# Kernel tuning notes

Measured on AMD Instinct MI355X. Metric: run time of the kernel, lower is better.

Reference implementation:

```python
import jax, jax.numpy as jnp
import numpy as np

N = 50000
E = 800000
IN_F = 128
HID_F = 128
OUT_F = 128
BN_EPS = 1e-5


def make_quaternion_mul(kernel):
    # kernel: [d_in//4, d_out]; returns hamilton: [d_in, d_out]
    r, i, j, k = jnp.split(kernel, 4, axis=1)
    r2 = jnp.concatenate([r, -i, -j, -k], axis=0)
    i2 = jnp.concatenate([i, r, -k, j], axis=0)
    j2 = jnp.concatenate([j, k, r, -i], axis=0)
    k2 = jnp.concatenate([k, -j, i, r], axis=0)
    return jnp.concatenate([r2, i2, j2, k2], axis=1)


def setup_inputs() -> dict:
    key = jax.random.key(0)
    k1, k2, k3, k4, k5, k6 = jax.random.split(key, 6)
    stdv = np.sqrt(6.0 / (IN_F // 4 + HID_F)).astype(np.float32)
    inputs = {
        "input": jax.random.normal(k1, (N, IN_F), dtype=jnp.float32),
        "adj_row": jnp.sort(jax.random.randint(k2, (E,), 0, N, dtype=jnp.int32)),
        "adj_col": jax.random.randint(k3, (E,), 0, N, dtype=jnp.int32),
        "adj_val": jax.random.uniform(k4, (E,), dtype=jnp.float32),
        "weight1": jax.random.uniform(k5, (IN_F // 4, HID_F), minval=-stdv, maxval=stdv, dtype=jnp.float32),
        "weight2": jax.random.uniform(k6, (HID_F // 4, OUT_F), minval=-stdv, maxval=stdv, dtype=jnp.float32),
        "gamma": jnp.ones((OUT_F,), dtype=jnp.float32),
        "beta": jnp.zeros((OUT_F,), dtype=jnp.float32),
    }
    return inputs


def reference(input, adj_row, adj_col, adj_val, weight1, weight2, gamma, beta):
    hamilton1 = make_quaternion_mul(weight1)  # [IN_F, HID_F]
    hamilton2 = make_quaternion_mul(weight2)  # [HID_F, OUT_F]
    out1 = jnp.tanh(input @ hamilton1)        # [N, HID_F]
    out2 = out1 @ hamilton2                   # [N, OUT_F]
    # sparse adj (COO) x dense: out[i] = sum_e val[e] * out2[col[e]] for row[e]==i
    gathered = adj_val[:, None] * out2[adj_col]  # [E, OUT_F]
    agg = jax.ops.segment_sum(gathered, adj_row, num_segments=N)  # [N, OUT_F]
    # BatchNorm1d (training mode): per-feature stats over nodes, biased var
    mean = jnp.mean(agg, axis=0)
    var = jnp.var(agg, axis=0)
    return gamma * (agg - mean) * jax.lax.rsqrt(var + BN_EPS) + beta
```

## Files before the change

kernel.cpp:

```cpp
#include <hip/hip_runtime.h>
#include <cstddef>
#include <cstdint>

#define F 128
#define LDK 136
#define AGG_BLOCKS 2048
#define MID_BLOCKS 64

typedef __attribute__((ext_vector_type(8))) short short8;
typedef __attribute__((ext_vector_type(4))) float f32x4;

__device__ __forceinline__ short f2bf(float f) {
  uint32_t u = __float_as_uint(f);
  uint32_t r = u + 0x7FFFu + ((u >> 16) & 1u);
  return (short)(r >> 16);
}
__device__ __forceinline__ float bf2f(short h) {
  return __uint_as_float(((uint32_t)(uint16_t)h) << 16);
}

__global__ __launch_bounds__(256) void setup_kernel(
    const float* __restrict__ w1, const float* __restrict__ w2,
    short* __restrict__ Hpk, const int* __restrict__ adj_row,
    const int* __restrict__ adj_col, const float* __restrict__ adj_val,
    int* __restrict__ rowptr, uint2* __restrict__ cv, int E, int N) {
  if (blockIdx.x < 16) {
    int idx = blockIdx.x * 256 + threadIdx.x;
    int m = idx >> 11;
    int kt = (idx >> 9) & 3;
    int ct = (idx >> 6) & 7;
    int l = idx & 63;
    int col = ct * 16 + (l & 15);
    const float* w = m ? w2 : w1;
    short hi[8], lo[8];
#pragma unroll
    for (int j = 0; j < 8; ++j) {
      int row = kt * 32 + (l >> 4) * 8 + j;
      int rb = row >> 5, cb = col >> 5;
      int neg = (0x284E >> (cb * 4 + rb)) & 1;
      float v = w[(row & 31) * 128 + (rb ^ cb) * 32 + (col & 31)];
      v = neg ? -v : v;
      short h = f2bf(v);
      hi[j] = h;
      lo[j] = f2bf(v - bf2f(h));
    }
    size_t b0 = ((((size_t)m * 2 + 0) * 4 + kt) * 8 + ct) * 64 + l;
    size_t b1 = ((((size_t)m * 2 + 1) * 4 + kt) * 8 + ct) * 64 + l;
    *(short8*)&Hpk[b0 * 8] = *(short8*)hi;
    *(short8*)&Hpk[b1 * 8] = *(short8*)lo;
  } else {
    int e = (blockIdx.x - 16) * 256 + threadIdx.x;
    if (e >= E) return;
    cv[e] = make_uint2((uint32_t)adj_col[e], __float_as_uint(adj_val[e]));
    int r = adj_row[e];
    int rprev = (e == 0) ? -1 : adj_row[e - 1];
    for (int q = rprev + 1; q <= r; ++q) rowptr[q] = e;
    if (e == E - 1) {
      for (int q = r + 1; q <= N; ++q) rowptr[q] = E;
    }
  }
}

__global__ __launch_bounds__(512) void gemm_mfma(
    const float* __restrict__ input, const short* __restrict__ Hpk,
    short* __restrict__ out2b, int N) {
  __shared__ short Hs[32768];
  __shared__ short lds[8][16 * LDK];
  const int t = threadIdx.x;
  const int w = t >> 6, l = t & 63;
  const int lr = l & 15, lg = l >> 4;
  const int grow0 = blockIdx.x * 128 + w * 16;
  short* hid = &lds[w][0];

#pragma unroll
  for (int i = 0; i < 8; ++i) {
    int idx = i * 512 + t;
    *(short8*)&Hs[idx * 8] = *(const short8*)&Hpk[idx * 8];
  }

  short8 a1h[4];
  {
    int arow = grow0 + lr;
    if (arow >= N) arow = N - 1;
    const float* xr = &input[(size_t)arow * F];
#pragma unroll
    for (int kt = 0; kt < 4; ++kt) {
      float xv[8];
      *(float4*)&xv[0] = *(const float4*)&xr[kt * 32 + lg * 8];
      *(float4*)&xv[4] = *(const float4*)&xr[kt * 32 + lg * 8 + 4];
#pragma unroll
      for (int j = 0; j < 8; ++j) ((short*)&a1h[kt])[j] = f2bf(xv[j]);
    }
  }
  __syncthreads();

  f32x4 acc[8];
#pragma unroll
  for (int ct = 0; ct < 8; ++ct) acc[ct] = (f32x4){0.f, 0.f, 0.f, 0.f};
#pragma unroll
  for (int kt = 0; kt < 4; ++kt) {
#pragma unroll
    for (int ct = 0; ct < 8; ++ct) {
      short8 bh = *(const short8*)&Hs[(((0 * 4 + kt) * 8 + ct) * 64 + l) * 8];
      short8 bl = *(const short8*)&Hs[(((1 * 4 + kt) * 8 + ct) * 64 + l) * 8];
      acc[ct] = __builtin_amdgcn_mfma_f32_16x16x32_bf16(a1h[kt], bl, acc[ct], 0, 0, 0);
      acc[ct] = __builtin_amdgcn_mfma_f32_16x16x32_bf16(a1h[kt], bh, acc[ct], 0, 0, 0);
    }
  }

#pragma unroll
  for (int ct = 0; ct < 8; ++ct)
#pragma unroll
    for (int r = 0; r < 4; ++r)
      hid[(lg * 4 + r) * LDK + ct * 16 + lr] = f2bf(tanhf(acc[ct][r]));

  short8 a2h[4];
#pragma unroll
  for (int kt = 0; kt < 4; ++kt)
    a2h[kt] = *(short8*)&hid[lr * LDK + kt * 32 + lg * 8];

  __syncthreads();
#pragma unroll
  for (int i = 0; i < 8; ++i) {
    int idx = i * 512 + t;
    *(short8*)&Hs[idx * 8] = *(const short8*)&Hpk[32768 + idx * 8];
  }
  __syncthreads();

#pragma unroll
  for (int ct = 0; ct < 8; ++ct) acc[ct] = (f32x4){0.f, 0.f, 0.f, 0.f};
#pragma unroll
  for (int kt = 0; kt < 4; ++kt) {
#pragma unroll
    for (int ct = 0; ct < 8; ++ct) {
      short8 bh = *(const short8*)&Hs[(((0 * 4 + kt) * 8 + ct) * 64 + l) * 8];
      short8 bl = *(const short8*)&Hs[(((1 * 4 + kt) * 8 + ct) * 64 + l) * 8];
      acc[ct] = __builtin_amdgcn_mfma_f32_16x16x32_bf16(a2h[kt], bl, acc[ct], 0, 0, 0);
      acc[ct] = __builtin_amdgcn_mfma_f32_16x16x32_bf16(a2h[kt], bh, acc[ct], 0, 0, 0);
    }
  }

#pragma unroll
  for (int ct = 0; ct < 8; ++ct)
#pragma unroll
    for (int r = 0; r < 4; ++r)
      hid[(lg * 4 + r) * LDK + ct * 16 + lr] = f2bf(acc[ct][r]);
#pragma unroll
  for (int i = 0; i < 4; ++i) {
    int chunk = i * 64 + l;
    int row = chunk >> 4, pos = chunk & 15;
    int grow = grow0 + row;
    if (grow < N)
      *(short8*)&out2b[(size_t)grow * F + pos * 8] = *(short8*)&hid[row * LDK + pos * 8];
  }
}

__global__ __launch_bounds__(256) void agg_rows7(
    const uint32_t* __restrict__ out2u,
    const int* __restrict__ rowptr, const uint2* __restrict__ cv,
    float* __restrict__ agg, float* __restrict__ partials, int N) {
  const int t = threadIdx.x;
  const int w = t >> 6, lane = t & 63;
  const int sub = lane >> 4;
  const int fl4 = (lane & 15) * 4;
  const int wid = blockIdx.x * 4 + w;
  const int nw = gridDim.x * 4;
  float ssum[8], ssq[8];
#pragma unroll
  for (int j = 0; j < 8; ++j) { ssum[j] = 0.f; ssq[j] = 0.f; }

  int pr = wid;
  bool active = pr * 2 < N;
  int sA = 0, eAe = 0, eBe = 0;
  if (active) {
    sA = rowptr[pr * 2];
    eAe = rowptr[pr * 2 + 1];
    eBe = (pr * 2 + 1 < N) ? rowptr[pr * 2 + 2] : eAe;
  }
  while (active) {
    const int prn = pr + nw;
    const bool actn = prn * 2 < N;
    int sAn = 0, eAen = 0, eBen = 0;
    if (actn) {
      sAn = rowptr[prn * 2];
      eAen = rowptr[prn * 2 + 1];
      eBen = (prn * 2 + 1 < N) ? rowptr[prn * 2 + 2] : eAen;
    }
    const int rowA = pr * 2;
    const bool hasB = rowA + 1 < N;
    const int sB = eAe;

    float accA[8], accB[8];
#pragma unroll
    for (int j = 0; j < 8; ++j) { accA[j] = 0.f; accB[j] = 0.f; }

    int eA = sA, eB = sB;
    while (eA < eAe || eB < eBe) {
      float vA[4], vB[4];
      uint32_t cA[4], cB[4];
#pragma unroll
      for (int q = 0; q < 4; ++q) {
        int ee = eA + q * 4 + sub;
        bool val = ee < eAe;
        int idx = val ? ee : (eAe - 1);
        idx = idx < 0 ? 0 : idx;
        uint2 p = cv[idx];
        cA[q] = p.x;
        vA[q] = val ? __uint_as_float(p.y) : 0.f;
      }
#pragma unroll
      for (int q = 0; q < 4; ++q) {
        int ee = eB + q * 4 + sub;
        bool val = ee < eBe;
        int idx = val ? ee : (eBe - 1);
        idx = idx < 0 ? 0 : idx;
        uint2 p = cv[idx];
        cB[q] = p.x;
        vB[q] = val ? __uint_as_float(p.y) : 0.f;
      }
      uint4 uA[4], uB[4];
#pragma unroll
      for (int q = 0; q < 4; ++q)
        uA[q] = *(const uint4*)&out2u[(size_t)(cA[q] * 64u + fl4)];
#pragma unroll
      for (int q = 0; q < 4; ++q)
        uB[q] = *(const uint4*)&out2u[(size_t)(cB[q] * 64u + fl4)];
#pragma unroll
      for (int q = 0; q < 4; ++q) {
#pragma unroll
        for (int k = 0; k < 4; ++k) {
          uint32_t ua = ((const uint32_t*)&uA[q])[k];
          uint32_t ub = ((const uint32_t*)&uB[q])[k];
          accA[2 * k]     = fmaf(vA[q], __uint_as_float(ua << 16), accA[2 * k]);
          accA[2 * k + 1] = fmaf(vA[q], __uint_as_float(ua & 0xFFFF0000u), accA[2 * k + 1]);
          accB[2 * k]     = fmaf(vB[q], __uint_as_float(ub << 16), accB[2 * k]);
          accB[2 * k + 1] = fmaf(vB[q], __uint_as_float(ub & 0xFFFF0000u), accB[2 * k + 1]);
        }
      }
      eA += 16;
      eB += 16;
    }
#pragma unroll
    for (int j = 0; j < 8; ++j) {
      accA[j] += __shfl_xor(accA[j], 16, 64);
      accA[j] += __shfl_xor(accA[j], 32, 64);
      accB[j] += __shfl_xor(accB[j], 16, 64);
      accB[j] += __shfl_xor(accB[j], 32, 64);
    }
    if (sub == 0) {
      *(float4*)&agg[(size_t)rowA * F + fl4 * 2] = make_float4(accA[0], accA[1], accA[2], accA[3]);
      *(float4*)&agg[(size_t)rowA * F + fl4 * 2 + 4] = make_float4(accA[4], accA[5], accA[6], accA[7]);
#pragma unroll
      for (int j = 0; j < 8; ++j) {
        ssum[j] += accA[j];
        ssq[j] = fmaf(accA[j], accA[j], ssq[j]);
      }
      if (hasB) {
        *(float4*)&agg[(size_t)(rowA + 1) * F + fl4 * 2] = make_float4(accB[0], accB[1], accB[2], accB[3]);
        *(float4*)&agg[(size_t)(rowA + 1) * F + fl4 * 2 + 4] = make_float4(accB[4], accB[5], accB[6], accB[7]);
#pragma unroll
        for (int j = 0; j < 8; ++j) {
          ssum[j] += accB[j];
          ssq[j] = fmaf(accB[j], accB[j], ssq[j]);
        }
      }
    }
    pr = prn;
    sA = sAn; eAe = eAen; eBe = eBen;
    active = actn;
  }

  __shared__ float ls[4][128];
  __shared__ float lq[4][128];
  if (sub == 0) {
#pragma unroll
    for (int j = 0; j < 8; ++j) {
      ls[w][fl4 * 2 + j] = ssum[j];
      lq[w][fl4 * 2 + j] = ssq[j];
    }
  }
  __syncthreads();
  if (t < 128) {
    float S = ls[0][t] + ls[1][t] + ls[2][t] + ls[3][t];
    float Q = lq[0][t] + lq[1][t] + lq[2][t] + lq[3][t];
    float* dst = &partials[(size_t)blockIdx.x * 256];
    dst[t] = S;
    dst[128 + t] = Q;
  }
}

__global__ __launch_bounds__(256) void mid_reduce(
    const float* __restrict__ partials, float* __restrict__ mid, int nb) {
  const int k = blockIdx.x, t = threadIdx.x;
  const int per = nb / MID_BLOCKS;
  float s = 0.f;
#pragma unroll 4
  for (int i = 0; i < per; ++i)
    s += partials[(size_t)(k * per + i) * 256 + t];
  mid[(size_t)k * 256 + t] = s;
}

__global__ __launch_bounds__(256) void finalize_stats3(
    const float* __restrict__ mid, const float* __restrict__ gamma,
    const float* __restrict__ beta, float* __restrict__ ss, float invN) {
  const int t = threadIdx.x;
  float s = 0.f;
#pragma unroll 8
  for (int b = 0; b < MID_BLOCKS; ++b) s += mid[(size_t)b * 256 + t];
  __shared__ float tot[256];
  tot[t] = s;
  __syncthreads();
  if (t < 128) {
    float mean = tot[t] * invN;
    float var = tot[128 + t] * invN - mean * mean;
    float inv = rsqrtf(var + 1e-5f);
    float sc = gamma[t] * inv;
    ss[t] = sc;
    ss[128 + t] = beta[t] - mean * sc;
  }
}

__global__ __launch_bounds__(256) void bn_apply(
    float* __restrict__ out, const float* __restrict__ ss, int total4) {
  int idx = blockIdx.x * 256 + threadIdx.x;
  if (idx >= total4) return;
  int f4 = (idx & 31) * 4;
  float4 v = *(float4*)&out[(size_t)idx * 4];
  float4 sc = *(const float4*)&ss[f4];
  float4 sh = *(const float4*)&ss[128 + f4];
  v.x = fmaf(v.x, sc.x, sh.x);
  v.y = fmaf(v.y, sc.y, sh.y);
  v.z = fmaf(v.z, sc.z, sh.z);
  v.w = fmaf(v.w, sc.w, sh.w);
  *(float4*)&out[(size_t)idx * 4] = v;
}

extern "C" void kernel_launch(void* const* d_in, const int* in_sizes, int n_in,
                              void* d_out, int out_size, void* d_ws, size_t ws_size,
                              hipStream_t stream) {
  (void)n_in; (void)out_size; (void)ws_size;
  const float* input  = (const float*)d_in[0];
  const int*  adj_row = (const int*)d_in[1];
  const int*  adj_col = (const int*)d_in[2];
  const float* adj_val = (const float*)d_in[3];
  const float* w1 = (const float*)d_in[4];
  const float* w2 = (const float*)d_in[5];
  const float* gamma = (const float*)d_in[6];
  const float* beta  = (const float*)d_in[7];
  const int N = in_sizes[0] / F;
  const int E = in_sizes[1];

  char* ws = (char*)d_ws;
  short* Hpk = (short*)(ws);
  float* ss = (float*)(ws + 131072);
  float* partials = (float*)(ws + 132096);
  float* mid = (float*)(ws + 2229248);
  int* rowptr = (int*)(ws + 2294784);
  uint2* cv = (uint2*)(ws + 2499584);
  size_t cv_bytes = ((size_t)E * 8 + 511) & ~(size_t)511;
  short* out2b = (short*)(ws + 2499584 + cv_bytes);
  float* agg = (float*)d_out;

  setup_kernel<<<16 + (E + 255) / 256, 256, 0, stream>>>(
      w1, w2, Hpk, adj_row, adj_col, adj_val, rowptr, cv, E, N);
  gemm_mfma<<<(N + 127) / 128, 512, 0, stream>>>(input, Hpk, out2b, N);
  agg_rows7<<<AGG_BLOCKS, 256, 0, stream>>>(
      (const uint32_t*)out2b, rowptr, cv, agg, partials, N);
  mid_reduce<<<MID_BLOCKS, 256, 0, stream>>>(partials, mid, AGG_BLOCKS);
  finalize_stats3<<<1, 256, 0, stream>>>(mid, gamma, beta, ss, 1.0f / (float)N);
  bn_apply<<<(N * 32 + 255) / 256, 256, 0, stream>>>(agg, ss, N * 32);
}
```

Before: 83.64 us.

## Halve GEMM block size and stage weight matrix in two LDS halves

The fused GEMM kernel now uses 256-thread blocks covering 64 rows instead of 512 threads covering 128. The Hamilton weight buffer in LDS is halved, so each weight matrix is staged and consumed in two K-halves with extra barriers. The aim is to cut LDS use per block so more blocks fit per CU and the grid has more blocks. The cost is twice as many weight-staging passes per output row and extra synchronisation.

```diff
diff --git a/kernel.cpp b/kernel.cpp
--- a/kernel.cpp
+++ b/kernel.cpp
@@ -61,21 +61,39 @@
   }
 }
 
-__global__ __launch_bounds__(512) void gemm_mfma(
+__global__ __launch_bounds__(256) void gemm_mfma(
     const float* __restrict__ input, const short* __restrict__ Hpk,
     short* __restrict__ out2b, int N) {
-  __shared__ short Hs[32768];
-  __shared__ short lds[8][16 * LDK];
+  __shared__ short Hs[16384];
+  __shared__ short lds[4][16 * LDK];
   const int t = threadIdx.x;
   const int w = t >> 6, l = t & 63;
   const int lr = l & 15, lg = l >> 4;
-  const int grow0 = blockIdx.x * 128 + w * 16;
+  const int grow0 = blockIdx.x * 64 + w * 16;
   short* hid = &lds[w][0];
 
-#pragma unroll
-  for (int i = 0; i < 8; ++i) {
-    int idx = i * 512 + t;
-    *(short8*)&Hs[idx * 8] = *(const short8*)&Hpk[idx * 8];
+#define STAGE_HALF(m, P)                                             \
+  {                                                                  \
+    const int base = ((m) * 8 + 2 * (P)) * 512;                      \
+    _Pragma("unroll") for (int i = 0; i < 8; ++i) {                  \
+      int idx = i * 256 + t;                                         \
+      int src = idx + base + (idx >> 10) * 1024;                     \
+      *(short8*)&Hs[idx * 8] = *(const short8*)&Hpk[src * 8];        \
+    }                                                                \
+  }
+
+#define GEMM_HALF(afrag, P)                                                          \
+  {                                                                                  \
+    _Pragma("unroll") for (int ktl = 0; ktl < 2; ++ktl) {                            \
+      _Pragma("unroll") for (int ct = 0; ct < 8; ++ct) {                             \
+        short8 bh = *(const short8*)&Hs[((ktl * 8 + ct) * 64 + l) * 8];              \
+        short8 bl = *(const short8*)&Hs[(((2 + ktl) * 8 + ct) * 64 + l) * 8];        \
+        acc[ct] = __builtin_amdgcn_mfma_f32_16x16x32_bf16(afrag[2 * (P) + ktl], bl,  \
+                                                          acc[ct], 0, 0, 0);         \
+        acc[ct] = __builtin_amdgcn_mfma_f32_16x16x32_bf16(afrag[2 * (P) + ktl], bh,  \
+                                                          acc[ct], 0, 0, 0);         \
+      }                                                                              \
+    }                                                                                \
   }
 
   short8 a1h[4];
@@ -92,21 +110,18 @@
       for (int j = 0; j < 8; ++j) ((short*)&a1h[kt])[j] = f2bf(xv[j]);
     }
   }
-  __syncthreads();
 
   f32x4 acc[8];
 #pragma unroll
   for (int ct = 0; ct < 8; ++ct) acc[ct] = (f32x4){0.f, 0.f, 0.f, 0.f};
-#pragma unroll
-  for (int kt = 0; kt < 4; ++kt) {
-#pragma unroll
-    for (int ct = 0; ct < 8; ++ct) {
-      short8 bh = *(const short8*)&Hs[(((0 * 4 + kt) * 8 + ct) * 64 + l) * 8];
-      short8 bl = *(const short8*)&Hs[(((1 * 4 + kt) * 8 + ct) * 64 + l) * 8];
-      acc[ct] = __builtin_amdgcn_mfma_f32_16x16x32_bf16(a1h[kt], bl, acc[ct], 0, 0, 0);
-      acc[ct] = __builtin_amdgcn_mfma_f32_16x16x32_bf16(a1h[kt], bh, acc[ct], 0, 0, 0);
-    }
-  }
+
+  STAGE_HALF(0, 0)
+  __syncthreads();
+  GEMM_HALF(a1h, 0)
+  __syncthreads();
+  STAGE_HALF(0, 1)
+  __syncthreads();
+  GEMM_HALF(a1h, 1)
 
 #pragma unroll
   for (int ct = 0; ct < 8; ++ct)
@@ -119,26 +134,17 @@
   for (int kt = 0; kt < 4; ++kt)
     a2h[kt] = *(short8*)&hid[lr * LDK + kt * 32 + lg * 8];
 
-  __syncthreads();
-#pragma unroll
-  for (int i = 0; i < 8; ++i) {
-    int idx = i * 512 + t;
-    *(short8*)&Hs[idx * 8] = *(const short8*)&Hpk[32768 + idx * 8];
-  }
-  __syncthreads();
-
 #pragma unroll
   for (int ct = 0; ct < 8; ++ct) acc[ct] = (f32x4){0.f, 0.f, 0.f, 0.f};
-#pragma unroll
-  for (int kt = 0; kt < 4; ++kt) {
-#pragma unroll
-    for (int ct = 0; ct < 8; ++ct) {
-      short8 bh = *(const short8*)&Hs[(((0 * 4 + kt) * 8 + ct) * 64 + l) * 8];
-      short8 bl = *(const short8*)&Hs[(((1 * 4 + kt) * 8 + ct) * 64 + l) * 8];
-      acc[ct] = __builtin_amdgcn_mfma_f32_16x16x32_bf16(a2h[kt], bl, acc[ct], 0, 0, 0);
-      acc[ct] = __builtin_amdgcn_mfma_f32_16x16x32_bf16(a2h[kt], bh, acc[ct], 0, 0, 0);
-    }
-  }
+
+  __syncthreads();
+  STAGE_HALF(1, 0)
+  __syncthreads();
+  GEMM_HALF(a2h, 0)
+  __syncthreads();
+  STAGE_HALF(1, 1)
+  __syncthreads();
+  GEMM_HALF(a2h, 1)
 
 #pragma unroll
   for (int ct = 0; ct < 8; ++ct)
@@ -153,6 +159,8 @@
     if (grow < N)
       *(short8*)&out2b[(size_t)grow * F + pos * 8] = *(short8*)&hid[row * LDK + pos * 8];
   }
+#undef STAGE_HALF
+#undef GEMM_HALF
 }
 
 __global__ __launch_bounds__(256) void agg_rows7(
@@ -363,7 +371,7 @@
 
   setup_kernel<<<16 + (E + 255) / 256, 256, 0, stream>>>(
       w1, w2, Hpk, adj_row, adj_col, adj_val, rowptr, cv, E, N);
-  gemm_mfma<<<(N + 127) / 128, 512, 0, stream>>>(input, Hpk, out2b, N);
+  gemm_mfma<<<(N + 63) / 64, 256, 0, stream>>>(input, Hpk, out2b, N);
   agg_rows7<<<AGG_BLOCKS, 256, 0, stream>>>(
       (const uint32_t*)out2b, rowptr, cv, agg, partials, N);
   mid_reduce<<<MID_BLOCKS, 256, 0, stream>>>(partials, mid, AGG_BLOCKS);
```

Measured after the change: 83.06 us. About the same (-0.7%).
